# Kernel optimization log

Measured on AMD Instinct MI355X. Metric: run time of the kernel, lower is better.

## Reference

```python
import jax, jax.numpy as jnp
import numpy as np

DIM = 256
NUM_HEADS = 8
HEAD_DIM = DIM // NUM_HEADS
Z_SHAPE = (32, 32)   # template grid -> qL = 1024
X_SHAPE = (64, 64)   # search grid  -> kvL = 4096
TBL = (max(Z_SHAPE[0], X_SHAPE[0]), max(Z_SHAPE[1], X_SHAPE[1]))  # (64, 64)
N_TABLE = (2 * TBL[0] - 1) * (2 * TBL[1] - 1)  # 16129


def _make_rel_index():
    """Faithful replication of the torch module's buffer construction (numpy, vectorized)."""
    H, W = TBL
    coords = np.stack(np.meshgrid(np.arange(H), np.arange(W), indexing='ij'), 0).reshape(2, -1)
    rel = coords[:, :, None] - coords[:, None, :]                     # (2, HW, HW)
    idx = (rel[0] + H - 1) * (2 * W - 1) + (rel[1] + W - 1)           # (HW, HW)
    h_z_begin = int(H / 2 - Z_SHAPE[0] / 2); h_x_begin = int(H / 2 - X_SHAPE[0] / 2)
    w_z_begin = int(W / 2 - Z_SHAPE[1] / 2); w_x_begin = int(W / 2 - X_SHAPE[1] / 2)
    hz = np.arange(h_z_begin, h_z_begin + Z_SHAPE[0])
    hx = np.arange(h_x_begin, h_x_begin + X_SHAPE[0])
    wz = np.arange(w_z_begin, w_z_begin + Z_SHAPE[1])
    wx = np.arange(w_x_begin, w_x_begin + X_SHAPE[1])
    # NOTE: source multiplies by z_2d_shape[0]/z_2d_shape[1] (kept faithfully, even though it looks odd)
    z_pos = hz[:, None] * Z_SHAPE[0] + wz[None, :]                    # (32, 32) axes (h_z, w_z)
    x_pos = hx[:, None] * Z_SHAPE[1] + wx[None, :]                    # (64, 64) axes (h_x, w_x)
    g = idx[z_pos][:, :, x_pos]                                       # (h_z, w_z, h_x, w_x)
    g = g.transpose(0, 2, 1, 3).reshape(Z_SHAPE[0] * Z_SHAPE[1], X_SHAPE[0] * X_SHAPE[1])
    return jnp.asarray(g, dtype=jnp.int32)                           # (qL, kvL)


def setup_inputs() -> dict:
    key = jax.random.key(0)
    ks = jax.random.split(key, 10)
    B, qL, kvL, C = 4, Z_SHAPE[0] * Z_SHAPE[1], X_SHAPE[0] * X_SHAPE[1], DIM
    return {
        'q': jax.random.normal(ks[0], (B, qL, C), jnp.float32),
        'kv': jax.random.normal(ks[1], (B, kvL, C), jnp.float32),
        'Wq': jax.random.normal(ks[2], (C, C), jnp.float32) * 0.02,
        'bq': jnp.zeros((C,), jnp.float32),
        'Wkv': jax.random.normal(ks[3], (2 * C, C), jnp.float32) * 0.02,
        'bkv': jnp.zeros((2 * C,), jnp.float32),
        'bias_table': jax.random.normal(ks[4], (N_TABLE, NUM_HEADS), jnp.float32) * 0.02,
        'Wp': jax.random.normal(ks[5], (C, C), jnp.float32) * 0.02,
        'bp': jnp.zeros((C,), jnp.float32),
        'rel_index': _make_rel_index(),
    }


def reference(q, kv, Wq, bq, Wkv, bkv, bias_table, Wp, bp, rel_index):
    B, qL, C = q.shape
    kvL = kv.shape[1]
    H, hd = NUM_HEADS, HEAD_DIM
    scale = hd ** (-0.5)
    Q = (q @ Wq.T + bq).reshape(B, qL, H, hd) * scale                  # bqhd
    KV = (kv @ Wkv.T + bkv).reshape(B, kvL, 2, H, hd)
    K, V = KV[:, :, 0], KV[:, :, 1]                                    # bkhd
    attn = jnp.einsum('bqhd,bkhd->bhqk', Q, K)                         # (B,H,qL,kvL)
    bias = bias_table[rel_index]                                       # (qL,kvL,H)
    attn = attn + jnp.transpose(bias, (2, 0, 1))[None]
    attn = jax.nn.softmax(attn, axis=-1)
    x = jnp.einsum('bhqk,bkhd->bqhd', attn, V).reshape(B, qL, C)
    return x @ Wp.T + bp
```

## Files before the change

### kernel.cpp

```cpp
#include <hip/hip_runtime.h>
#include <math.h>

#define DIM 256
#define NUM_HEADS 8
#define HEAD_DIM 32
#define QL 1024
#define KVL 4096
#define BATCH 4
#define NTAB 16129
#define LOG2E 1.4426950408889634f

typedef __attribute__((ext_vector_type(8))) short short8;
typedef __attribute__((ext_vector_type(4))) float floatx4;
typedef __attribute__((ext_vector_type(4))) unsigned short ushort4v;

__device__ inline unsigned short f2bf(float x) {
    unsigned u = __builtin_bit_cast(unsigned, x);
    unsigned r = (u + 0x7FFFu + ((u >> 16) & 1u)) >> 16;
    return (unsigned short)r;
}
__device__ inline float bf2f(unsigned short h) {
    return __builtin_bit_cast(float, (unsigned)h << 16);
}
__device__ inline floatx4 mfma16(short8 a, short8 b, floatx4 c) {
    return __builtin_amdgcn_mfma_f32_16x16x32_bf16(a, b, c, 0, 0, 0);
}

__global__ __launch_bounds__(256) void split_all(
    const float* __restrict__ q, const float* __restrict__ kv,
    const float* __restrict__ Wq, const float* __restrict__ Wkv,
    const float* __restrict__ Wp, const float* __restrict__ bias_table,
    unsigned short* __restrict__ qh, unsigned short* __restrict__ kvh,
    unsigned short* __restrict__ Wqh, unsigned short* __restrict__ Wkvh,
    unsigned short* __restrict__ Wph, unsigned short* __restrict__ Wpl,
    float* __restrict__ Bt)
{
    const int gid = blockIdx.x * 256 + threadIdx.x;
    if (gid >= 1408514) return;
    if (gid >= 1376256) {
        const int local = gid - 1376256;
        const float4 v = ((const float4*)bias_table)[local];
        const float vv[4] = {v.x, v.y, v.z, v.w};
        const int base = local * 4;
#pragma unroll
        for (int j = 0; j < 4; ++j) {
            const int i = (base + j) >> 3, h = (base + j) & 7;
            Bt[h * NTAB + i] = vv[j] * LOG2E;
        }
        return;
    }
    const float* src; unsigned short* dh; unsigned short* dl = nullptr; int local;
    if (gid < 262144)       { src = q;   dh = qh;   local = gid; }
    else if (gid < 1310720) { src = kv;  dh = kvh;  local = gid - 262144; }
    else if (gid < 1327104) { src = Wq;  dh = Wqh;  local = gid - 1310720; }
    else if (gid < 1359872) { src = Wkv; dh = Wkvh; local = gid - 1327104; }
    else                    { src = Wp;  dh = Wph;  dl = Wpl; local = gid - 1359872; }
    const float4 v = ((const float4*)src)[local];
    ushort4v h;
    h[0] = f2bf(v.x); h[1] = f2bf(v.y); h[2] = f2bf(v.z); h[3] = f2bf(v.w);
    ((ushort4v*)dh)[local] = h;
    if (dl) {
        ushort4v l;
        l[0] = f2bf(v.x - bf2f(h[0])); l[1] = f2bf(v.y - bf2f(h[1]));
        l[2] = f2bf(v.z - bf2f(h[2])); l[3] = f2bf(v.w - bf2f(h[3]));
        ((ushort4v*)dl)[local] = l;
    }
}

template<int MODE, int BW>
__device__ __forceinline__ void gemm_core(
    const unsigned short* __restrict__ Ah, const unsigned short* __restrict__ Al,
    const unsigned short* __restrict__ Wh, const unsigned short* __restrict__ Wl,
    const float* __restrict__ bias, float* __restrict__ Cf,
    unsigned short* __restrict__ Cb, float scale, int bx, int by)
{
    constexpr bool THREE = (MODE == 0);
    const int t    = threadIdx.x;
    const int w    = t >> 6;
    const int lane = t & 63;
    const int n16  = lane & 15;
    const int quad = lane >> 4;
    const int m0 = by * (BW * 32) + w * 32;
    const int n0 = bx * 64;

    floatx4 acc[2][4];
#pragma unroll
    for (int s = 0; s < 2; ++s)
#pragma unroll
        for (int c = 0; c < 4; ++c) acc[s][c] = (floatx4){0.f, 0.f, 0.f, 0.f};

    short8 af[2][2], afl[2][2], wf[2][4], wfl[2][4];

    auto LD = [&](int kb, int bi) {
#pragma unroll
        for (int s = 0; s < 2; ++s) {
            af[bi][s] = *(const short8*)(Ah + (size_t)(m0 + s * 16 + n16) * 256 + kb + quad * 8);
            if (THREE)
                afl[bi][s] = *(const short8*)(Al + (size_t)(m0 + s * 16 + n16) * 256 + kb + quad * 8);
        }
#pragma unroll
        for (int c = 0; c < 4; ++c) {
            wf[bi][c] = *(const short8*)(Wh + (size_t)(n0 + c * 16 + n16) * 256 + kb + quad * 8);
            if (THREE)
                wfl[bi][c] = *(const short8*)(Wl + (size_t)(n0 + c * 16 + n16) * 256 + kb + quad * 8);
        }
    };

    LD(0, 0);
#pragma unroll
    for (int i = 0; i < 8; ++i) {
        const int cur = i & 1, nxt = cur ^ 1;
        if (i < 7) LD((i + 1) * 32, nxt);
#pragma unroll
        for (int c = 0; c < 4; ++c)
#pragma unroll
            for (int s = 0; s < 2; ++s) {
                acc[s][c] = mfma16(af[cur][s], wf[cur][c], acc[s][c]);
                if (THREE) {
                    acc[s][c] = mfma16(af[cur][s], wfl[cur][c], acc[s][c]);
                    acc[s][c] = mfma16(afl[cur][s], wf[cur][c], acc[s][c]);
                }
            }
    }

#pragma unroll
    for (int s = 0; s < 2; ++s)
#pragma unroll
        for (int c = 0; c < 4; ++c) {
            const floatx4 v = acc[s][c];
            const int n_g = n0 + c * 16 + n16;
#pragma unroll
            for (int r = 0; r < 4; ++r) {
                const int m_g = m0 + s * 16 + quad * 4 + r;
                const float val = v[r];
                if (MODE == 0) {
                    Cf[(size_t)m_g * 256 + n_g] = val + bias[n_g];
                } else if (MODE == 1) {
                    const int h = n_g >> 5, d = n_g & 31;
                    const int b = m_g >> 10, qq = m_g & 1023;
                    Cb[(((size_t)(b * 8 + h) * 1024 + qq) << 5) + d] =
                        f2bf((val + bias[n_g]) * scale);
                } else if (MODE == 2) {
                    const int h = n_g >> 5, d = n_g & 31;
                    const int b = m_g >> 12, kvr = m_g & 4095;
                    Cb[(((size_t)(b * 8 + h) * 4096 + kvr) << 5) + d] =
                        f2bf(val + bias[n_g]);
                } else {
                    const int h = m_g >> 5, dd = m_g & 31;
                    const int b = n_g >> 12, kvr = n_g & 4095;
                    Cb[(((size_t)((b * 8 + h) * 32 + dd)) << 12) + kvr] =
                        f2bf(val + bias[m_g]);
                }
            }
        }
}

__global__ __launch_bounds__(256) void gemm_qkv(
    const unsigned short* __restrict__ qh, const unsigned short* __restrict__ kvh,
    const unsigned short* __restrict__ Wqh, const unsigned short* __restrict__ Wkvh,
    const float* __restrict__ bq, const float* __restrict__ bkv,
    unsigned short* __restrict__ Qb, unsigned short* __restrict__ Kb,
    unsigned short* __restrict__ Vt, float scale)
{
    const int id = blockIdx.x;
    if (id < 128) {
        gemm_core<1, 4>(qh, nullptr, Wqh, nullptr, bq, nullptr, Qb, scale,
                        id & 3, id >> 2);
    } else if (id < 640) {
        const int t2 = id - 128;
        gemm_core<2, 4>(kvh, nullptr, Wkvh, nullptr, bkv, nullptr, Kb, 1.0f,
                        t2 & 3, t2 >> 2);
    } else {
        const int t2 = id - 640;
        gemm_core<3, 4>(Wkvh + 256 * 256, nullptr, kvh, nullptr, bkv + 256,
                        nullptr, Vt, 1.0f, t2 >> 1, t2 & 1);
    }
}

__global__ __launch_bounds__(128) void gemm_out(
    const unsigned short* __restrict__ Xh, const unsigned short* __restrict__ Xl,
    const unsigned short* __restrict__ Wph, const unsigned short* __restrict__ Wpl,
    const float* __restrict__ bp, float* __restrict__ out)
{
    gemm_core<0, 2>(Xh, Xl, Wph, Wpl, bp, out, nullptr, 1.0f,
                    blockIdx.x, blockIdx.y);
}

__global__ __launch_bounds__(256, 3) void attn_mfma(
    const unsigned short* __restrict__ Qb,
    const unsigned short* __restrict__ Kb,
    const unsigned short* __restrict__ Vt,
    const float* __restrict__ Bt,
    float* __restrict__ Op,
    float* __restrict__ lp)
{
    const int id   = blockIdx.x;
    const int qt   = id >> 7;
    const int rest = id & 127;
    const int h    = rest & 7;
    const int sp   = (rest >> 3) & 3;
    const int b    = rest >> 5;
    const int bh = b * NUM_HEADS + h;
    const int tid  = threadIdx.x;
    const int w    = tid >> 6;
    const int lane = tid & 63;
    const int n    = lane & 15;
    const int quad = lane >> 4;

    __shared__ __align__(16) unsigned short Ps[4][16 * 72];

    const int qrowA = qt * 64 + w * 16 + n;
    const short8 qf = *(const short8*)(Qb + (((size_t)bh * QL + qrowA) << 5) + quad * 8);

    const int qgC = qt * 64 + w * 16 + quad * 4;
    const float* Bth = Bt + h * NTAB;

    const int vS = sp >> 1;
    int ivals[4], B0r[4];
#pragma unroll
    for (int r = 0; r < 4; ++r) {
        const int q = qgC + r;
        ivals[r] = q >> 5;
        B0r[r]   = (((q & 31) << 1) + vS) << 5;
    }

    floatx4 o0 = {0.f, 0.f, 0.f, 0.f};
    floatx4 o1 = {0.f, 0.f, 0.f, 0.f};
    float lacc[4] = {0.f, 0.f, 0.f, 0.f};

    const unsigned short* Kbase = Kb + (((size_t)bh * KVL) << 5);
    const unsigned short* Vbase = Vt + (((size_t)bh * 32) << 12);
    const int kbase = sp * 1024;

    short8 kf[2][4];
    float  bv[2][16];

    auto LDK = [&](int kt, int bi) {
        const int kv0 = kbase + kt * 64;
#pragma unroll
        for (int c = 0; c < 4; ++c)
            kf[bi][c] = *(const short8*)(Kbase + ((size_t)(kv0 + c * 16 + n) << 5) + quad * 8);
    };
    auto GATHER = [&](int kt, int bi) {
        const int jS = ((sp << 4) + kt) & 31;
#pragma unroll
        for (int r = 0; r < 4; ++r) {
            const int a  = 528 + (ivals[r] << 5) + jS;
            const int A0 = ((a >> 6) + 63) * 127 + (a & 63) + 63;
#pragma unroll
            for (int c = 0; c < 4; ++c) {
                const int bb  = B0r[r] + c * 16 + n;
                const int idx = A0 - ((bb >> 6) * 127 + (bb & 63));
                bv[bi][r * 4 + c] = Bth[idx];
            }
        }
    };

    LDK(0, 0);
    GATHER(0, 0);

#pragma unroll
    for (int kt = 0; kt < 16; ++kt) {
        const int cur = kt & 1, nxt = cur ^ 1;
        const int kv0 = kbase + kt * 64;

        short8 vf[2][2];
#pragma unroll
        for (int kc = 0; kc < 2; ++kc)
#pragma unroll
            for (int dh = 0; dh < 2; ++dh)
                vf[kc][dh] = *(const short8*)(Vbase + ((size_t)(dh * 16 + n) << 12)
                                              + kv0 + kc * 32 + quad * 8);

        floatx4 sc[4];
#pragma unroll
        for (int c = 0; c < 4; ++c) {
            floatx4 z = {0.f, 0.f, 0.f, 0.f};
            sc[c] = mfma16(qf, kf[cur][c], z);
        }

        if (kt < 15) { LDK(kt + 1, nxt); GATHER(kt + 1, nxt); }

#pragma unroll
        for (int r = 0; r < 4; ++r)
#pragma unroll
            for (int c = 0; c < 4; ++c) {
                const float p = exp2f(fmaf(sc[c][r], LOG2E, bv[cur][r * 4 + c]));
                lacc[r] += p;
                Ps[w][(quad * 4 + r) * 72 + c * 16 + n] = f2bf(p);
            }
        asm volatile("s_waitcnt lgkmcnt(0)" ::: "memory");

#pragma unroll
        for (int kc = 0; kc < 2; ++kc) {
            const short8 pf = *(const short8*)(Ps[w] + n * 72 + kc * 32 + quad * 8);
            o0 = mfma16(pf, vf[kc][0], o0);
            o1 = mfma16(pf, vf[kc][1], o1);
        }
        asm volatile("" ::: "memory");
    }

#pragma unroll
    for (int r = 0; r < 4; ++r) {
        float v = lacc[r];
        v += __shfl_xor(v, 1, 16);
        v += __shfl_xor(v, 2, 16);
        v += __shfl_xor(v, 4, 16);
        v += __shfl_xor(v, 8, 16);
        lacc[r] = v;
    }

    float* Opb = Op + (((size_t)(sp * 32 + bh) * QL) << 5);
#pragma unroll
    for (int r = 0; r < 4; ++r) {
        const int qg = qgC + r;
        Opb[((size_t)qg << 5) + n]      = o0[r];
        Opb[((size_t)qg << 5) + 16 + n] = o1[r];
    }
    if (n == 0) {
        float* lpb = lp + (size_t)(sp * 32 + bh) * QL;
#pragma unroll
        for (int r = 0; r < 4; ++r) lpb[qgC + r] = lacc[r];
    }
}

__global__ __launch_bounds__(256) void attn_combine(
    const float* __restrict__ Op, const float* __restrict__ lp,
    unsigned short* __restrict__ Xh, unsigned short* __restrict__ Xl)
{
    const int gid = blockIdx.x * 256 + threadIdx.x;
    const int bhq = gid >> 5, d = gid & 31;
    const int bh = bhq >> 10, q = bhq & 1023;
    const int b = bh >> 3, hh = bh & 7;
    float o = 0.f, l = 0.f;
#pragma unroll
    for (int s = 0; s < 4; ++s) {
        o += Op[((size_t)(s * 32768 + bhq) << 5) + d];
        l += lp[s * 32768 + bhq];
    }
    const float val = o / l;
    const size_t idx = ((size_t)(b * QL + q)) * DIM + hh * HEAD_DIM + d;
    const unsigned short h = f2bf(val);
    Xh[idx] = h;
    Xl[idx] = f2bf(val - bf2f(h));
}

extern "C" void kernel_launch(void* const* d_in, const int* in_sizes, int n_in,
                              void* d_out, int out_size, void* d_ws, size_t ws_size,
                              hipStream_t stream)
{
    const float* q          = (const float*)d_in[0];
    const float* kv         = (const float*)d_in[1];
    const float* Wq         = (const float*)d_in[2];
    const float* bq         = (const float*)d_in[3];
    const float* Wkv        = (const float*)d_in[4];
    const float* bkv        = (const float*)d_in[5];
    const float* bias_table = (const float*)d_in[6];
    const float* Wp         = (const float*)d_in[7];
    const float* bp         = (const float*)d_in[8];
    float* out = (float*)d_out;

    char* ws = (char*)d_ws;
    unsigned short* Qb   = (unsigned short*)(ws);
    unsigned short* Kb   = (unsigned short*)(ws + (size_t)(2u  << 20));
    unsigned short* Vt   = (unsigned short*)(ws + (size_t)(10u << 20));
    unsigned short* kvh  = (unsigned short*)(ws + (size_t)(18u << 20));
    float*          Op   = (float*)         (ws + (size_t)(18u << 20));
    float*          lp   = (float*)         (ws + (size_t)(34u << 20));
    float*          Bt   = (float*)         (ws + (size_t)(34u << 20) + (512u << 10));
    unsigned short* qh   = (unsigned short*)(ws + (size_t)(36u << 20));
    unsigned short* Wqh  = (unsigned short*)(ws + (size_t)(38u << 20));
    unsigned short* Wkvh = (unsigned short*)(ws + (size_t)(38u << 20) + (128u << 10));
    unsigned short* Wph  = (unsigned short*)(ws + (size_t)(38u << 20) + (384u << 10));
    unsigned short* Wpl  = (unsigned short*)(ws + (size_t)(38u << 20) + (512u << 10));
    unsigned short* Xh   = qh;
    unsigned short* Xl   = Vt;

    const float scale = 1.0f / sqrtf((float)HEAD_DIM);

    split_all<<<dim3(5503), 256, 0, stream>>>(q, kv, Wq, Wkv, Wp, bias_table,
                                              qh, kvh, Wqh, Wkvh, Wph, Wpl, Bt);
    gemm_qkv<<<dim3(1152), 256, 0, stream>>>(qh, kvh, Wqh, Wkvh, bq, bkv,
                                             Qb, Kb, Vt, scale);
    attn_mfma<<<dim3(2048), 256, 0, stream>>>(Qb, Kb, Vt, Bt, Op, lp);
    attn_combine<<<dim3(4096), 256, 0, stream>>>(Op, lp, Xh, Xl);
    gemm_out<<<dim3(4, 64), 128, 0, stream>>>(Xh, Xl, Wph, Wpl, bp, out);
}
```

Measured before the change: 246.1 us.

## Fuse fp32-to-bf16 conversion into QKV GEMM loads and drop split kernel

Removes the separate split_all conversion pass. The QKV projection GEMM now reads fp32 q, kv and weights directly and converts them to bf16 in registers as it loads. The Wp hi/lo split and the bias-table transpose move into extra blocks of the same launch. This saves one kernel launch and the write-then-reread of the bf16 copies of q and kv, but the GEMM now loads twice as many bytes per fragment and repeats the conversion for each tile that reuses an input row.

Measured after the change: 267.2 us. 8.6% more time.

```diff
diff --git a/kernel.cpp b/kernel.cpp
--- a/kernel.cpp
+++ b/kernel.cpp
@@ -25,52 +25,21 @@
 __device__ inline floatx4 mfma16(short8 a, short8 b, floatx4 c) {
     return __builtin_amdgcn_mfma_f32_16x16x32_bf16(a, b, c, 0, 0, 0);
 }
-
-__global__ __launch_bounds__(256) void split_all(
-    const float* __restrict__ q, const float* __restrict__ kv,
-    const float* __restrict__ Wq, const float* __restrict__ Wkv,
-    const float* __restrict__ Wp, const float* __restrict__ bias_table,
-    unsigned short* __restrict__ qh, unsigned short* __restrict__ kvh,
-    unsigned short* __restrict__ Wqh, unsigned short* __restrict__ Wkvh,
-    unsigned short* __restrict__ Wph, unsigned short* __restrict__ Wpl,
-    float* __restrict__ Bt)
-{
-    const int gid = blockIdx.x * 256 + threadIdx.x;
-    if (gid >= 1408514) return;
-    if (gid >= 1376256) {
-        const int local = gid - 1376256;
-        const float4 v = ((const float4*)bias_table)[local];
-        const float vv[4] = {v.x, v.y, v.z, v.w};
-        const int base = local * 4;
-#pragma unroll
-        for (int j = 0; j < 4; ++j) {
-            const int i = (base + j) >> 3, h = (base + j) & 7;
-            Bt[h * NTAB + i] = vv[j] * LOG2E;
-        }
-        return;
-    }
-    const float* src; unsigned short* dh; unsigned short* dl = nullptr; int local;
-    if (gid < 262144)       { src = q;   dh = qh;   local = gid; }
-    else if (gid < 1310720) { src = kv;  dh = kvh;  local = gid - 262144; }
-    else if (gid < 1327104) { src = Wq;  dh = Wqh;  local = gid - 1310720; }
-    else if (gid < 1359872) { src = Wkv; dh = Wkvh; local = gid - 1327104; }
-    else                    { src = Wp;  dh = Wph;  dl = Wpl; local = gid - 1359872; }
-    const float4 v = ((const float4*)src)[local];
-    ushort4v h;
-    h[0] = f2bf(v.x); h[1] = f2bf(v.y); h[2] = f2bf(v.z); h[3] = f2bf(v.w);
-    ((ushort4v*)dh)[local] = h;
-    if (dl) {
-        ushort4v l;
-        l[0] = f2bf(v.x - bf2f(h[0])); l[1] = f2bf(v.y - bf2f(h[1]));
-        l[2] = f2bf(v.z - bf2f(h[2])); l[3] = f2bf(v.w - bf2f(h[3]));
-        ((ushort4v*)dl)[local] = l;
-    }
-}
-
-template<int MODE, int BW>
+__device__ inline short8 cvt8(const float* p) {
+    const float4 a = *(const float4*)p;
+    const float4 b = *(const float4*)(p + 4);
+    short8 r;
+    r[0] = (short)f2bf(a.x); r[1] = (short)f2bf(a.y);
+    r[2] = (short)f2bf(a.z); r[3] = (short)f2bf(a.w);
+    r[4] = (short)f2bf(b.x); r[5] = (short)f2bf(b.y);
+    r[6] = (short)f2bf(b.z); r[7] = (short)f2bf(b.w);
+    return r;
+}
+
+template<int MODE, int BW, bool INF32>
 __device__ __forceinline__ void gemm_core(
-    const unsigned short* __restrict__ Ah, const unsigned short* __restrict__ Al,
-    const unsigned short* __restrict__ Wh, const unsigned short* __restrict__ Wl,
+    const void* __restrict__ A_, const void* __restrict__ Al_,
+    const void* __restrict__ W_, const void* __restrict__ Wl_,
     const float* __restrict__ bias, float* __restrict__ Cf,
     unsigned short* __restrict__ Cb, float scale, int bx, int by)
 {
@@ -94,15 +63,19 @@
     auto LD = [&](int kb, int bi) {
 #pragma unroll
         for (int s = 0; s < 2; ++s) {
-            af[bi][s] = *(const short8*)(Ah + (size_t)(m0 + s * 16 + n16) * 256 + kb + quad * 8);
+            const size_t off = (size_t)(m0 + s * 16 + n16) * 256 + kb + quad * 8;
+            if (INF32) af[bi][s] = cvt8((const float*)A_ + off);
+            else       af[bi][s] = *(const short8*)((const unsigned short*)A_ + off);
             if (THREE)
-                afl[bi][s] = *(const short8*)(Al + (size_t)(m0 + s * 16 + n16) * 256 + kb + quad * 8);
+                afl[bi][s] = *(const short8*)((const unsigned short*)Al_ + off);
         }
 #pragma unroll
         for (int c = 0; c < 4; ++c) {
-            wf[bi][c] = *(const short8*)(Wh + (size_t)(n0 + c * 16 + n16) * 256 + kb + quad * 8);
+            const size_t off = (size_t)(n0 + c * 16 + n16) * 256 + kb + quad * 8;
+            if (INF32) wf[bi][c] = cvt8((const float*)W_ + off);
+            else       wf[bi][c] = *(const short8*)((const unsigned short*)W_ + off);
             if (THREE)
-                wfl[bi][c] = *(const short8*)(Wl + (size_t)(n0 + c * 16 + n16) * 256 + kb + quad * 8);
+                wfl[bi][c] = *(const short8*)((const unsigned short*)Wl_ + off);
         }
     };
 
@@ -155,25 +128,51 @@
         }
 }
 
-__global__ __launch_bounds__(256) void gemm_qkv(
-    const unsigned short* __restrict__ qh, const unsigned short* __restrict__ kvh,
-    const unsigned short* __restrict__ Wqh, const unsigned short* __restrict__ Wkvh,
+__global__ __launch_bounds__(256) void gemm_qkv_prep(
+    const float* __restrict__ q, const float* __restrict__ kv,
+    const float* __restrict__ Wq, const float* __restrict__ Wkv,
+    const float* __restrict__ Wp, const float* __restrict__ bias_table,
     const float* __restrict__ bq, const float* __restrict__ bkv,
     unsigned short* __restrict__ Qb, unsigned short* __restrict__ Kb,
-    unsigned short* __restrict__ Vt, float scale)
+    unsigned short* __restrict__ Vt,
+    unsigned short* __restrict__ Wph, unsigned short* __restrict__ Wpl,
+    float* __restrict__ Bt, float scale)
 {
     const int id = blockIdx.x;
     if (id < 128) {
-        gemm_core<1, 4>(qh, nullptr, Wqh, nullptr, bq, nullptr, Qb, scale,
-                        id & 3, id >> 2);
+        gemm_core<1, 4, true>(q, nullptr, Wq, nullptr, bq, nullptr, Qb, scale,
+                              id & 3, id >> 2);
     } else if (id < 640) {
         const int t2 = id - 128;
-        gemm_core<2, 4>(kvh, nullptr, Wkvh, nullptr, bkv, nullptr, Kb, 1.0f,
-                        t2 & 3, t2 >> 2);
+        gemm_core<2, 4, true>(kv, nullptr, Wkv, nullptr, bkv, nullptr, Kb, 1.0f,
+                              t2 & 3, t2 >> 2);
+    } else if (id < 1152) {
+        const int t2 = id - 640;
+        gemm_core<3, 4, true>(Wkv + 256 * 256, nullptr, kv, nullptr, bkv + 256,
+                              nullptr, Vt, 1.0f, t2 >> 1, t2 & 1);
     } else {
-        const int t2 = id - 640;
-        gemm_core<3, 4>(Wkvh + 256 * 256, nullptr, kvh, nullptr, bkv + 256,
-                        nullptr, Vt, 1.0f, t2 >> 1, t2 & 1);
+        const int gid = (id - 1152) * 256 + threadIdx.x;
+        if (gid < 16384) {
+            const float4 v = ((const float4*)Wp)[gid];
+            ushort4v h, l;
+            h[0] = f2bf(v.x); h[1] = f2bf(v.y); h[2] = f2bf(v.z); h[3] = f2bf(v.w);
+            l[0] = f2bf(v.x - bf2f(h[0])); l[1] = f2bf(v.y - bf2f(h[1]));
+            l[2] = f2bf(v.z - bf2f(h[2])); l[3] = f2bf(v.w - bf2f(h[3]));
+            ((ushort4v*)Wph)[gid] = h;
+            ((ushort4v*)Wpl)[gid] = l;
+        } else {
+            const int g2 = gid - 16384;
+            if (g2 < 32258) {
+                const float4 v = ((const float4*)bias_table)[g2];
+                const float vv[4] = {v.x, v.y, v.z, v.w};
+                const int base = g2 * 4;
+#pragma unroll
+                for (int j = 0; j < 4; ++j) {
+                    const int i = (base + j) >> 3, h = (base + j) & 7;
+                    Bt[h * NTAB + i] = vv[j] * LOG2E;
+                }
+            }
+        }
     }
 }
 
@@ -182,8 +181,8 @@
     const unsigned short* __restrict__ Wph, const unsigned short* __restrict__ Wpl,
     const float* __restrict__ bp, float* __restrict__ out)
 {
-    gemm_core<0, 2>(Xh, Xl, Wph, Wpl, bp, out, nullptr, 1.0f,
-                    blockIdx.x, blockIdx.y);
+    gemm_core<0, 2, false>(Xh, Xl, Wph, Wpl, bp, out, nullptr, 1.0f,
+                           blockIdx.x, blockIdx.y);
 }
 
 __global__ __launch_bounds__(256, 3) void attn_mfma(
@@ -364,24 +363,19 @@
     unsigned short* Qb   = (unsigned short*)(ws);
     unsigned short* Kb   = (unsigned short*)(ws + (size_t)(2u  << 20));
     unsigned short* Vt   = (unsigned short*)(ws + (size_t)(10u << 20));
-    unsigned short* kvh  = (unsigned short*)(ws + (size_t)(18u << 20));
     float*          Op   = (float*)         (ws + (size_t)(18u << 20));
     float*          lp   = (float*)         (ws + (size_t)(34u << 20));
     float*          Bt   = (float*)         (ws + (size_t)(34u << 20) + (512u << 10));
-    unsigned short* qh   = (unsigned short*)(ws + (size_t)(36u << 20));
-    unsigned short* Wqh  = (unsigned short*)(ws + (size_t)(38u << 20));
-    unsigned short* Wkvh = (unsigned short*)(ws + (size_t)(38u << 20) + (128u << 10));
+    unsigned short* Xh   = (unsigned short*)(ws + (size_t)(36u << 20));
     unsigned short* Wph  = (unsigned short*)(ws + (size_t)(38u << 20) + (384u << 10));
     unsigned short* Wpl  = (unsigned short*)(ws + (size_t)(38u << 20) + (512u << 10));
-    unsigned short* Xh   = qh;
     unsigned short* Xl   = Vt;
 
     const float scale = 1.0f / sqrtf((float)HEAD_DIM);
 
-    split_all<<<dim3(5503), 256, 0, stream>>>(q, kv, Wq, Wkv, Wp, bias_table,
-                                              qh, kvh, Wqh, Wkvh, Wph, Wpl, Bt);
-    gemm_qkv<<<dim3(1152), 256, 0, stream>>>(qh, kvh, Wqh, Wkvh, bq, bkv,
-                                             Qb, Kb, Vt, scale);
+    gemm_qkv_prep<<<dim3(1344), 256, 0, stream>>>(
+        q, kv, Wq, Wkv, Wp, bias_table, bq, bkv,
+        Qb, Kb, Vt, Wph, Wpl, Bt, scale);
     attn_mfma<<<dim3(2048), 256, 0, stream>>>(Qb, Kb, Vt, Bt, Op, lp);
     attn_combine<<<dim3(4096), 256, 0, stream>>>(Op, lp, Xh, Xl);
     gemm_out<<<dim3(4, 64), 128, 0, stream>>>(Xh, Xl, Wph, Wpl, bp, out);
```
